# Optimization experiments

Measured on AMD Instinct MI355X. Metric: run time of the kernel, lower is better.

## Reference

```python
import jax, jax.numpy as jnp
import numpy as np

B, L_IN, D = 4, 4096, 1024
R_MIN, R_MAX = 0.9, 0.999


def setup_inputs() -> dict:
    key = jax.random.key(0)
    k0, k1, k2 = jax.random.split(key, 3)
    inputs = jax.random.normal(k0, (B, L_IN, D), jnp.float32)
    Wi = jax.random.normal(k1, (2 * D, D), jnp.float32) / np.sqrt(D)
    bi = jnp.zeros((2 * D,), jnp.float32)
    Wo = jax.random.normal(k2, (D, 2 * D), jnp.float32) / np.sqrt(2 * D)
    bo = jnp.zeros((D,), jnp.float32)
    # LRU stable-ring initialization, exactly as in the torch module
    rng = np.random.default_rng(0)
    u1 = rng.random(D)
    u2 = rng.random(D)
    v_log = np.log(-0.5 * np.log(u1 * (R_MAX ** 2 - R_MIN ** 2) + R_MIN ** 2))
    theta_log = np.log(u2 * np.pi * 2)
    gamma_log = np.log(np.sqrt(1.0 - np.exp(-np.exp(v_log)) ** 2))
    params_log = jnp.asarray(np.stack([v_log, theta_log, gamma_log]), jnp.float32)
    return {"inputs": inputs, "Wi": Wi, "bi": bi, "Wo": Wo, "bo": bo,
            "params_log": params_log}


def _lru_forward(inputs, Wi, bi, Wo, bo, params_log):
    b, l_in, d = inputs.shape
    u = inputs @ Wi.T + bi                      # [B, L, 2D]
    v, theta, gamma = jnp.exp(params_log)       # each [D]
    # torch.view_as_complex: interleaved (real, imag) pairs along last dim
    uc = u.reshape(b, l_in, d, 2)
    x = jax.lax.complex(uc[..., 0], uc[..., 1])  # [B, L, D] complex64
    log2_L = int(np.ceil(np.log2(l_in)))
    L = 2 ** log2_L
    x = jnp.pad(x, ((0, 0), (0, L - l_in), (0, 0)))
    # Blelloch-style log-depth scan: x_t = lambda * x_{t-1} + u_t,
    # lambda = exp(-v + i*theta)
    for i in range(1, log2_L + 1):
        blk = 2 ** i
        xb = x.reshape(b * L // blk, blk, d)
        x1, x2 = xb[:, : blk // 2], xb[:, blk // 2:]
        pos = jnp.arange(1, blk // 2 + 1, dtype=jnp.float32)  # [blk/2]
        lambs = jnp.exp(jax.lax.complex(-pos[:, None] * v,
                                        pos[:, None] * theta))  # [blk/2, D]
        x2 = x2 + lambs * x1[:, -1:]
        x = jnp.concatenate([x1, x2], axis=1).reshape(b, L, d)
    x = x[:, :l_in] * gamma.astype(x.dtype)     # normalize, drop padding
    xr = jnp.concatenate([x.real, x.imag], axis=-1)  # [B, L, 2D]
    out = xr @ Wo.T + bo
    return jax.nn.relu(out)


def reference(inputs, Wi, bi, Wo, bo, params_log):
    return _lru_forward(inputs, Wi, bi, Wo, bo, params_log)
```

## Files before the change

### kernel.cpp

```cpp
#include <hip/hip_runtime.h>

#define BB 4
#define LL 4096
#define DD 1024
#define SS 64
#define TT 64

typedef __attribute__((ext_vector_type(4))) float  floatx4;
typedef __attribute__((ext_vector_type(8))) short  shortx8;

static __device__ __forceinline__ unsigned short f2bf(float f) {
    unsigned int u = __float_as_uint(f);
    u += 0x7fffu + ((u >> 16) & 1u);
    return (unsigned short)(u >> 16);
}
static __device__ __forceinline__ float bf2f(unsigned short h) {
    return __uint_as_float(((unsigned int)h) << 16);
}

#define NIN4 (BB * LL * DD / 4)
#define NW4  (2 * DD * DD / 4)
__global__ void cast_all_kernel(const float4* __restrict__ s_in, ushort4* __restrict__ d_inb,
                                const float4* __restrict__ s_wi, ushort4* __restrict__ d_wib,
                                const float4* __restrict__ s_wo, ushort4* __restrict__ d_wob) {
    int i = blockIdx.x * blockDim.x + threadIdx.x;
    const float4* s; ushort4* d; int j;
    if (i < NIN4)                 { s = s_in; d = d_inb; j = i; }
    else if (i < NIN4 + NW4)      { s = s_wi; d = d_wib; j = i - NIN4; }
    else                          { s = s_wo; d = d_wob; j = i - NIN4 - NW4; }
    float4 v = s[j];
    ushort4 o;
    o.x = f2bf(v.x); o.y = f2bf(v.y); o.z = f2bf(v.z); o.w = f2bf(v.w);
    d[j] = o;
}

template<int K, int NT, int EPI>
__global__ __launch_bounds__(512, 2)
void gemm256(const unsigned short* __restrict__ A,
             const unsigned short* __restrict__ B,
             const float* __restrict__ bias,
             void* __restrict__ Cp) {
    constexpr int N   = NT * 256;
    constexpr int NKT = K / 64;
    __shared__ __align__(16) short As[2][256 * 64];
    __shared__ __align__(16) short Bs[2][256 * 64];

    const int tid = threadIdx.x;
    const int blk = blockIdx.x;
    const int xcd = blk & 7;
    const int i2  = blk >> 3;
    const int tileM = ((i2 / NT) * 8 + xcd) * 256;
    const int tileN = (i2 % NT) * 256;

    const int lane   = tid & 63;
    const int wave   = tid >> 6;
    const int wave_m = wave >> 2;
    const int wave_n = wave & 3;
    const int r16    = lane & 15;
    const int quad   = lane >> 4;
    const int slotx  = r16 & 7;
    const int wmRow  = wave_m * 64 + r16;
    const int wnRow  = wave_n * 32 + r16;

    const int srow = tid >> 3;
    const int scol = ((tid & 7) ^ (srow & 7)) * 8;
    const int ldsChunkBase = (tid & ~63) * 8;
    const size_t aOff = (size_t)(tileM + srow) * K + scol;
    const size_t bOff = (size_t)(tileN + srow) * K + scol;

    floatx4 acc[8][4] = {};
    shortx8 af[4][2], bf0v[2][2], bf1v[2][2];

#define GLL(SRC, DST) __builtin_amdgcn_global_load_lds( \
        (const __attribute__((address_space(1))) void*)(SRC), \
        (__attribute__((address_space(3))) void*)(DST), 16, 0, 0)
#define STAGE_A(BUF, H, KT) do { \
    GLL(A + aOff + (size_t)((H) * 128) * K + (KT) * 64,      &As[BUF][(H) * 8192 + ldsChunkBase]); \
    GLL(A + aOff + (size_t)((H) * 128 + 64) * K + (KT) * 64, &As[BUF][(H) * 8192 + 4096 + ldsChunkBase]); \
} while (0)
#define STAGE_B(BUF, H, KT) do { \
    GLL(B + bOff + (size_t)((H) * 128) * K + (KT) * 64,      &Bs[BUF][(H) * 8192 + ldsChunkBase]); \
    GLL(B + bOff + (size_t)((H) * 128 + 64) * K + (KT) * 64, &Bs[BUF][(H) * 8192 + 4096 + ldsChunkBase]); \
} while (0)
#define LOAD_A(BUF, MH) do { \
    _Pragma("unroll") for (int il = 0; il < 4; ++il) \
    _Pragma("unroll") for (int kk = 0; kk < 2; ++kk) \
        af[il][kk] = *(const shortx8*)&As[BUF][((MH) * 128 + wmRow + il * 16) * 64 + ((kk * 4 + quad) ^ slotx) * 8]; \
} while (0)
#define LOAD_B(BUF, NH, DST) do { \
    _Pragma("unroll") for (int jl = 0; jl < 2; ++jl) \
    _Pragma("unroll") for (int kk = 0; kk < 2; ++kk) \
        DST[jl][kk] = *(const shortx8*)&Bs[BUF][((NH) * 128 + wnRow + jl * 16) * 64 + ((kk * 4 + quad) ^ slotx) * 8]; \
} while (0)
#define MFMAQ(MH, NH, BF) do { \
    __builtin_amdgcn_s_setprio(1); \
    _Pragma("unroll") for (int kk = 0; kk < 2; ++kk) \
    _Pragma("unroll") for (int il = 0; il < 4; ++il) \
    _Pragma("unroll") for (int jl = 0; jl < 2; ++jl) \
        acc[(MH) * 4 + il][(NH) * 2 + jl] = __builtin_amdgcn_mfma_f32_16x16x32_bf16( \
            af[il][kk], BF[jl][kk], acc[(MH) * 4 + il][(NH) * 2 + jl], 0, 0, 0); \
    __builtin_amdgcn_s_setprio(0); \
} while (0)

    STAGE_A(0, 0, 0);
    STAGE_B(0, 0, 0);
    STAGE_B(0, 1, 0);
    STAGE_A(0, 1, 0);
    STAGE_A(1, 0, 1);
    STAGE_B(1, 1, 1);
    STAGE_A(1, 1, 1);
    asm volatile("s_waitcnt vmcnt(6)" ::: "memory");
    __builtin_amdgcn_s_barrier();

    for (int t = 0; t < NKT; ++t) {
        const int cb = t & 1;
        const int t1 = (t + 1 < NKT) ? t + 1 : NKT - 1;
        const int t2 = (t + 2 < NKT) ? t + 2 : NKT - 1;
        LOAD_A(cb, 0);
        LOAD_B(cb, 0, bf0v);
        STAGE_B(cb ^ 1, 0, t1);
        __builtin_amdgcn_s_barrier();
        asm volatile("s_waitcnt lgkmcnt(0)" ::: "memory");
        MFMAQ(0, 0, bf0v);
        __builtin_amdgcn_s_barrier();
        LOAD_B(cb, 1, bf1v);
        STAGE_A(cb, 0, t2);
        __builtin_amdgcn_s_barrier();
        asm volatile("s_waitcnt lgkmcnt(0)" ::: "memory");
        MFMAQ(0, 1, bf1v);
        __builtin_amdgcn_s_barrier();
        LOAD_A(cb, 1);
        STAGE_B(cb, 1, t2);
        __builtin_amdgcn_s_barrier();
        asm volatile("s_waitcnt lgkmcnt(0)" ::: "memory");
        MFMAQ(1, 0, bf0v);
        __builtin_amdgcn_s_barrier();
        STAGE_A(cb, 1, t2);
        asm volatile("s_waitcnt vmcnt(6)" ::: "memory");
        __builtin_amdgcn_s_barrier();
        MFMAQ(1, 1, bf1v);
        __builtin_amdgcn_s_barrier();
    }
    asm volatile("s_waitcnt vmcnt(0)" ::: "memory");

#pragma unroll
    for (int i = 0; i < 8; ++i) {
        const int row0 = tileM + (i >> 2) * 128 + wave_m * 64 + (i & 3) * 16 + quad * 4;
#pragma unroll
        for (int j = 0; j < 4; ++j) {
            const int col = tileN + (j >> 1) * 128 + wave_n * 32 + (j & 1) * 16 + r16;
            const float bv = bias[col];
#pragma unroll
            for (int r = 0; r < 4; ++r) {
                float v = acc[i][j][r] + bv;
                if (EPI == 0) {
                    ((unsigned short*)Cp)[(size_t)(row0 + r) * N + col] = f2bf(v);
                } else {
                    ((float*)Cp)[(size_t)(row0 + r) * N + col] = fmaxf(v, 0.0f);
                }
            }
        }
    }
#undef GLL
#undef STAGE_A
#undef STAGE_B
#undef LOAD_A
#undef LOAD_B
#undef MFMAQ
}

__global__ __launch_bounds__(256)
void scanA(const unsigned short* __restrict__ u,
           const float* __restrict__ plog,
           float2* __restrict__ Eend) {
    const int d0 = (blockIdx.x * 256 + threadIdx.x) * 2;
    const int c = blockIdx.y, b = blockIdx.z;
    const float v0  = expf(plog[d0]),      v1  = expf(plog[d0 + 1]);
    const float th0 = expf(plog[DD + d0]), th1 = expf(plog[DD + d0 + 1]);
    const float a0 = expf(-v0), a1 = expf(-v1);
    const float lr0 = a0 * cosf(th0), li0 = a0 * sinf(th0);
    const float lr1 = a1 * cosf(th1), li1 = a1 * sinf(th1);
    float zr0 = 0.f, zi0 = 0.f, zr1 = 0.f, zi1 = 0.f;
    const unsigned short* up = u + (size_t)(b * LL + c * TT) * (2 * DD) + 2 * d0;
#pragma unroll 4
    for (int tl = 0; tl < TT; ++tl) {
        uint2 pr = *(const uint2*)up;
        float xr0 = bf2f((unsigned short)(pr.x & 0xffffu));
        float xi0 = bf2f((unsigned short)(pr.x >> 16));
        float xr1 = bf2f((unsigned short)(pr.y & 0xffffu));
        float xi1 = bf2f((unsigned short)(pr.y >> 16));
        float t;
        t = lr0 * zr0 - li0 * zi0 + xr0; zi0 = lr0 * zi0 + li0 * zr0 + xi0; zr0 = t;
        t = lr1 * zr1 - li1 * zi1 + xr1; zi1 = lr1 * zi1 + li1 * zr1 + xi1; zr1 = t;
        up += 2 * DD;
    }
    *(float4*)&Eend[(size_t)c * (BB * DD) + b * DD + d0] =
        make_float4(zr0, zi0, zr1, zi1);
}

__global__ __launch_bounds__(256)
void scanC(const unsigned short* __restrict__ u,
           const float* __restrict__ plog,
           const float2* __restrict__ Eend,
           unsigned short* __restrict__ xr) {
    const int d0 = (blockIdx.x * 256 + threadIdx.x) * 2;
    const int c = blockIdx.y, b = blockIdx.z;
    const float v0  = expf(plog[d0]),      v1  = expf(plog[d0 + 1]);
    const float th0 = expf(plog[DD + d0]), th1 = expf(plog[DD + d0 + 1]);
    const float g0  = expf(plog[2 * DD + d0]), g1 = expf(plog[2 * DD + d0 + 1]);
    const float a0 = expf(-v0), a1 = expf(-v1);
    const float lr0 = a0 * cosf(th0), li0 = a0 * sinf(th0);
    const float lr1 = a1 * cosf(th1), li1 = a1 * sinf(th1);

    const float aT0 = expf(-(float)TT * v0), aT1 = expf(-(float)TT * v1);
    const float Lr0 = aT0 * cosf((float)TT * th0), Li0 = aT0 * sinf((float)TT * th0);
    const float Lr1 = aT1 * cosf((float)TT * th1), Li1 = aT1 * sinf((float)TT * th1);
    float yr0 = 0.f, yi0 = 0.f, yr1 = 0.f, yi1 = 0.f;
    for (int cc = 0; cc < c; ++cc) {
        float4 e = *(const float4*)&Eend[(size_t)cc * (BB * DD) + b * DD + d0];
        float t;
        t = Lr0 * yr0 - Li0 * yi0 + e.x; yi0 = Lr0 * yi0 + Li0 * yr0 + e.y; yr0 = t;
        t = Lr1 * yr1 - Li1 * yi1 + e.z; yi1 = Lr1 * yi1 + Li1 * yr1 + e.w; yr1 = t;
    }

    const unsigned short* up = u + (size_t)(b * LL + c * TT) * (2 * DD) + 2 * d0;
    unsigned short* xp = xr + (size_t)(b * LL + c * TT) * (2 * DD) + d0;
#pragma unroll 4
    for (int tl = 0; tl < TT; ++tl) {
        uint2 pr = *(const uint2*)up;
        float xr0 = bf2f((unsigned short)(pr.x & 0xffffu));
        float xi0 = bf2f((unsigned short)(pr.x >> 16));
        float xr1 = bf2f((unsigned short)(pr.y & 0xffffu));
        float xi1 = bf2f((unsigned short)(pr.y >> 16));
        float t;
        t = lr0 * yr0 - li0 * yi0 + xr0; yi0 = lr0 * yi0 + li0 * yr0 + xi0; yr0 = t;
        t = lr1 * yr1 - li1 * yi1 + xr1; yi1 = lr1 * yi1 + li1 * yr1 + xi1; yr1 = t;
        *(unsigned int*)&xp[0]  = (unsigned int)f2bf(g0 * yr0) |
                                  ((unsigned int)f2bf(g1 * yr1) << 16);
        *(unsigned int*)&xp[DD] = (unsigned int)f2bf(g0 * yi0) |
                                  ((unsigned int)f2bf(g1 * yi1) << 16);
        up += 2 * DD;
        xp += 2 * DD;
    }
}

extern "C" void kernel_launch(void* const* d_in, const int* in_sizes, int n_in,
                              void* d_out, int out_size, void* d_ws, size_t ws_size,
                              hipStream_t stream) {
    const float* inputs = (const float*)d_in[0];
    const float* Wi     = (const float*)d_in[1];
    const float* bi     = (const float*)d_in[2];
    const float* Wo     = (const float*)d_in[3];
    const float* bo     = (const float*)d_in[4];
    const float* plog   = (const float*)d_in[5];
    float* out = (float*)d_out;

    const size_t M = (size_t)BB * LL;
    unsigned short* u_bf  = (unsigned short*)d_ws;
    unsigned short* xr_bf = u_bf  + M * 2 * DD;
    unsigned short* in_bf = xr_bf + M * 2 * DD;
    unsigned short* Wi_bf = in_bf + M * DD;
    unsigned short* Wo_bf = Wi_bf + (size_t)2 * DD * DD;
    float2* Eend = (float2*)(Wo_bf + (size_t)2 * DD * DD);

    {
        int total4 = NIN4 + 2 * NW4;
        cast_all_kernel<<<total4 / 256, 256, 0, stream>>>(
            (const float4*)inputs, (ushort4*)in_bf,
            (const float4*)Wi,     (ushort4*)Wi_bf,
            (const float4*)Wo,     (ushort4*)Wo_bf);
    }

    gemm256<DD, 8, 0><<<(M / 256) * 8, 512, 0, stream>>>(
        in_bf, Wi_bf, bi, (void*)u_bf);

    scanA<<<dim3(DD / 512, SS, BB), 256, 0, stream>>>(u_bf, plog, Eend);
    scanC<<<dim3(DD / 512, SS, BB), 256, 0, stream>>>(u_bf, plog, Eend, xr_bf);

    gemm256<2 * DD, 4, 1><<<(M / 256) * 4, 512, 0, stream>>>(
        xr_bf, Wo_bf, bo, (void*)out);
}
```

Before: 306.2 us.

## Restructure GEMM main loop to overlap LDS fragment loads with MFMA

Restructures the pipelined bf16 GEMM main loop so each LDS fragment load is issued before the preceding MFMA block instead of after a barrier. The first A/B fragments of the next k-tile are prefetched at the end of the current iteration. The barrier count per iteration drops from eight to four, the vmcnt wait moves earlier, and the loop is unrolled by two. This is meant to hide LDS latency and barrier stalls behind matrix math, at the risk of correctness hazards in the reordered buffer reuse and higher register pressure.

```diff
diff --git a/kernel.cpp b/kernel.cpp
--- a/kernel.cpp
+++ b/kernel.cpp
@@ -101,6 +101,8 @@
             af[il][kk], BF[jl][kk], acc[(MH) * 4 + il][(NH) * 2 + jl], 0, 0, 0); \
     __builtin_amdgcn_s_setprio(0); \
 } while (0)
+#define BAR()  __builtin_amdgcn_s_barrier()
+#define LGKM0() asm volatile("s_waitcnt lgkmcnt(0)" ::: "memory")
 
     STAGE_A(0, 0, 0);
     STAGE_B(0, 0, 0);
@@ -110,38 +112,37 @@
     STAGE_B(1, 1, 1);
     STAGE_A(1, 1, 1);
     asm volatile("s_waitcnt vmcnt(6)" ::: "memory");
-    __builtin_amdgcn_s_barrier();
-
+    BAR();
+    LOAD_A(0, 0);
+    LOAD_B(0, 0, bf0v);
+
+#pragma unroll 2
     for (int t = 0; t < NKT; ++t) {
         const int cb = t & 1;
         const int t1 = (t + 1 < NKT) ? t + 1 : NKT - 1;
         const int t2 = (t + 2 < NKT) ? t + 2 : NKT - 1;
-        LOAD_A(cb, 0);
-        LOAD_B(cb, 0, bf0v);
+        BAR();
+        LGKM0();
         STAGE_B(cb ^ 1, 0, t1);
-        __builtin_amdgcn_s_barrier();
-        asm volatile("s_waitcnt lgkmcnt(0)" ::: "memory");
         MFMAQ(0, 0, bf0v);
-        __builtin_amdgcn_s_barrier();
         LOAD_B(cb, 1, bf1v);
+        BAR();
+        LGKM0();
         STAGE_A(cb, 0, t2);
-        __builtin_amdgcn_s_barrier();
-        asm volatile("s_waitcnt lgkmcnt(0)" ::: "memory");
         MFMAQ(0, 1, bf1v);
-        __builtin_amdgcn_s_barrier();
         LOAD_A(cb, 1);
+        BAR();
+        LGKM0();
         STAGE_B(cb, 1, t2);
-        __builtin_amdgcn_s_barrier();
-        asm volatile("s_waitcnt lgkmcnt(0)" ::: "memory");
         MFMAQ(1, 0, bf0v);
-        __builtin_amdgcn_s_barrier();
+        asm volatile("s_waitcnt vmcnt(4)" ::: "memory");
+        BAR();
         STAGE_A(cb, 1, t2);
-        asm volatile("s_waitcnt vmcnt(6)" ::: "memory");
-        __builtin_amdgcn_s_barrier();
         MFMAQ(1, 1, bf1v);
-        __builtin_amdgcn_s_barrier();
-    }
-    asm volatile("s_waitcnt vmcnt(0)" ::: "memory");
+        LOAD_A(cb ^ 1, 0);
+        LOAD_B(cb ^ 1, 0, bf0v);
+    }
+    asm volatile("s_waitcnt vmcnt(0) lgkmcnt(0)" ::: "memory");
 
 #pragma unroll
     for (int i = 0; i < 8; ++i) {
@@ -167,6 +168,8 @@
 #undef LOAD_A
 #undef LOAD_B
 #undef MFMAQ
+#undef BAR
+#undef LGKM0
 }
 
 __global__ __launch_bounds__(256)
```

New measurement: 305.1 us. Within noise of the previous version (-0.4%).
